# Performance work log

Measured on AMD Instinct MI355X. Metric: run time of the kernel, lower is better.

The kernel has to match this reference:

```python
import jax, jax.numpy as jnp
import numpy as np


def setup_inputs() -> dict:
    key = jax.random.key(0)
    k_z, k_cb = jax.random.split(key)
    B, S, D, K = 8, 4096, 256, 8192
    z = jax.random.normal(k_z, (B, S, D), dtype=jnp.float32)
    codebook = jax.random.normal(k_cb, (K, D), dtype=jnp.float32)
    return {"z": z, "codebook": codebook}


def reference(z, codebook):
    """BaseVectorQuantizer.get_quants with distance_type='square',
    padding_idx=-1 (disabled), prob_decay=0 (deterministic argmin).

    z: (B, S, D); codebook: (K, D).
    Returns (embedding (B, S, D), q_indices (B, S, 1)).

    Squared L2 distance uses the ||z||^2 + ||e||^2 - 2 z e^T expansion
    (same math as the broadcasted (z - e)^2 sum, but GEMM-based).
    """
    B, S, D = z.shape
    zf = z.reshape(-1, D)                               # (N, D), N = B*S
    z_sq = jnp.sum(zf * zf, axis=-1, keepdims=True)     # (N, 1)
    e_sq = jnp.sum(codebook * codebook, axis=-1)        # (K,)
    # (N, K) squared distances
    dist = z_sq + e_sq[None, :] - 2.0 * jnp.einsum("nd,kd->nk", zf, codebook)
    idx = jnp.argmin(dist, axis=1)                      # (N,)
    embedding = jnp.take(codebook, idx, axis=0).reshape(B, S, D)
    q_indices = idx.reshape(B, S, 1)
    return embedding, q_indices
```

## Files before the change

### kernel.cpp

```cpp
#include <hip/hip_runtime.h>

constexpr int D  = 256;
constexpr int K  = 8192;
constexpr int N  = 32768;

typedef _Float16 f16;
typedef f16   f16x8  __attribute__((ext_vector_type(8)));
typedef float f32x16 __attribute__((ext_vector_type(16)));

__device__ __forceinline__ void gload_lds16(const void* g, void* l) {
    __builtin_amdgcn_global_load_lds(
        (const __attribute__((address_space(1))) unsigned int*)g,
        (__attribute__((address_space(3))) unsigned int*)l,
        16, 0, 0);
}


__global__ void esq_kernel(const float* __restrict__ cb, float* __restrict__ esq) {
    const int lane = threadIdx.x & 63;
    const int code = (int)((blockIdx.x * (size_t)blockDim.x + threadIdx.x) >> 6);
    const float4 v = *reinterpret_cast<const float4*>(cb + (size_t)code * D + lane * 4);
    float s = v.x * v.x + v.y * v.y + v.z * v.z + v.w * v.w;
    #pragma unroll
    for (int m = 32; m >= 1; m >>= 1) s += __shfl_xor(s, m);
    if (lane == 0) esq[code] = s;
}

__global__ void cvt_t(const float* __restrict__ cb, f16* __restrict__ cbt) {
    const int g    = blockIdx.x * 256 + threadIdx.x;
    const int s    = g >> 13;
    const int code = g & 8191;
    const float* src = cb + (size_t)code * D + (s & 31) * 8;
    const float4 a  = *reinterpret_cast<const float4*>(src);
    const float4 b2 = *reinterpret_cast<const float4*>(src + 4);
    const float vf[8] = {a.x, a.y, a.z, a.w, b2.x, b2.y, b2.z, b2.w};
    f16x8 o;
    if (s < 32) {
        #pragma unroll
        for (int e = 0; e < 8; ++e) o[e] = (f16)vf[e];
    } else {
        #pragma unroll
        for (int e = 0; e < 8; ++e) {
            f16 h = (f16)vf[e];
            o[e] = (f16)((vf[e] - (float)h) * 1024.0f);
        }
    }
    *reinterpret_cast<f16x8*>(cbt + ((size_t)s * 8192 + code) * 8) = o;
}

__launch_bounds__(256, 2)
__global__ void vq32(const float* __restrict__ z, const f16* __restrict__ cbt,
                     const float* __restrict__ esq,
                     float* __restrict__ wsv, int* __restrict__ wsi) {
    __shared__ f16 buf[2][16384];

    const int tid  = threadIdx.x;
    const int w    = tid >> 6;
    const int l    = tid & 63;
    const int cid  = l & 31;
    const int half = l >> 5;
    const int rg    = blockIdx.x >> 1;
    const int kh    = blockIdx.x & 1;
    const int kbase = kh * 4096;
    const size_t wrow0 = (size_t)rg * 128 + w * 32;

    f16x8 zh[16], zl[16];
    {
        const float* zr = z + (wrow0 + cid) * D + half * 8;
        #pragma unroll
        for (int u = 0; u < 16; ++u) {
            float4 a  = *reinterpret_cast<const float4*>(zr + u * 16);
            float4 b2 = *reinterpret_cast<const float4*>(zr + u * 16 + 4);
            float vf[8] = {a.x, a.y, a.z, a.w, b2.x, b2.y, b2.z, b2.w};
            f16x8 h, lo;
            #pragma unroll
            for (int e = 0; e < 8; ++e) {
                f16 hh = (f16)vf[e];
                h[e]  = hh;
                lo[e] = (f16)((vf[e] - (float)hh) * 1024.0f);
            }
            zh[u] = h; zl[u] = lo;
        }
    }

    float minv[16];
    int   mini[16];
    #pragma unroll
    for (int g = 0; g < 16; ++g) { minv[g] = 3.0e38f; mini[g] = 0; }

    f32x16 accA = (f32x16)0.0f, accB = (f32x16)0.0f;

    #pragma unroll
    for (int j = 0; j < 8; ++j) {
        const int s = w * 16 + 2 * j + half;
        gload_lds16(cbt + ((size_t)s * 8192 + kbase + cid) * 8,
                    &buf[0][(w * 16 + 2 * j) * 256]);
    }
    __syncthreads();

    for (int kt = 0; kt < 128; ++kt) {
        const int  b        = kt & 1;
        const bool haveNext = (kt < 127);

        if (haveNext) {
            const int k0n = kbase + (kt + 1) * 32;
            #pragma unroll
            for (int j = 0; j < 8; ++j) {
                const int s = w * 16 + 2 * j + half;
                gload_lds16(cbt + ((size_t)s * 8192 + k0n + cid) * 8,
                            &buf[b ^ 1][(w * 16 + 2 * j) * 256]);
            }
        }
        const float es = esq[kbase + kt * 32 + cid];

        const f16* Bp = &buf[b][0];
        __builtin_amdgcn_s_setprio(1);
        #pragma unroll
        for (int u = 0; u < 16; ++u) {
            f16x8 beh = *reinterpret_cast<const f16x8*>(Bp + ((2 * u + half) * 32 + cid) * 8);
            f16x8 bel = *reinterpret_cast<const f16x8*>(Bp + ((32 + 2 * u + half) * 32 + cid) * 8);
            accA = __builtin_amdgcn_mfma_f32_32x32x16_f16(zh[u], beh, accA, 0, 0, 0);
            accB = __builtin_amdgcn_mfma_f32_32x32x16_f16(zl[u], beh, accB, 0, 0, 0);
            accB = __builtin_amdgcn_mfma_f32_32x32x16_f16(zh[u], bel, accB, 0, 0, 0);
        }
        __builtin_amdgcn_s_setprio(0);

        const int c0 = kbase + kt * 32 + cid;
        #pragma unroll
        for (int g = 0; g < 16; ++g) {
            float d = fmaf(accB[g], 0.0009765625f, accA[g]);
            float s = fmaf(-2.0f, d, es);
            if (s < minv[g]) { minv[g] = s; mini[g] = c0; }
        }
        accA = (f32x16)0.0f; accB = (f32x16)0.0f;

        if (haveNext) __syncthreads();
    }

    #pragma unroll
    for (int g = 0; g < 16; ++g) {
        float v   = minv[g];
        int   idx = mini[g];
        #pragma unroll
        for (int m = 1; m < 32; m <<= 1) {
            float ov = __shfl_xor(v, m);
            int   oi = __shfl_xor(idx, m);
            if (ov < v || (ov == v && oi < idx)) { v = ov; idx = oi; }
        }
        const size_t row = wrow0 + (g & 3) + 8 * (g >> 2) + 4 * half;
        if (cid == 0) {
            wsv[(size_t)kh * N + row] = v;
            wsi[(size_t)kh * N + row] = idx;
        }
    }
}

__global__ void merge_gather(const float* __restrict__ wsv, const int* __restrict__ wsi,
                             const float* __restrict__ cb, float* __restrict__ out) {
    const int t   = threadIdx.x;
    const int r   = blockIdx.x * 16 + (t >> 4);
    const int l16 = t & 15;
    const float v0 = wsv[r], v1 = wsv[N + r];
    const int   i0 = wsi[r], i1 = wsi[N + r];
    const int idx = (v1 < v0) ? i1 : i0;
    if (l16 == 0) out[(size_t)N * D + r] = (float)idx;
    const float4* src = reinterpret_cast<const float4*>(cb + (size_t)idx * D);
    float4*       dst = reinterpret_cast<float4*>(out + (size_t)r * D);
    #pragma unroll
    for (int it = 0; it < 4; ++it) dst[l16 + 16 * it] = src[l16 + 16 * it];
}

constexpr int BM = 128, BN = 128, TD = 32, ZS = 260, CS = 36;

__launch_bounds__(256)
__global__ void vq_kernel(const float* __restrict__ z, const float* __restrict__ cb,
                          const float* __restrict__ esq, float* __restrict__ out) {
    __shared__ float zs[BM * ZS];
    __shared__ float cs[BN * CS];
    const int tid = threadIdx.x;
    const int tx  = tid & 15;
    const int ty  = tid >> 4;
    const size_t row0 = (size_t)blockIdx.x * BM;
    #pragma unroll
    for (int i = 0; i < 32; ++i) {
        int f  = tid + i * 256;
        int r  = f >> 6;
        int c4 = (f & 63) * 4;
        *reinterpret_cast<float4*>(&zs[r * ZS + c4]) =
            *reinterpret_cast<const float4*>(z + (row0 + r) * D + c4);
    }
    float minv[8]; int mini[8];
    #pragma unroll
    for (int i = 0; i < 8; ++i) { minv[i] = 3.4e38f; mini[i] = 0; }
    for (int k0 = 0; k0 < K; k0 += BN) {
        float acc[8][8];
        #pragma unroll
        for (int i = 0; i < 8; ++i)
            #pragma unroll
            for (int j = 0; j < 8; ++j) acc[i][j] = 0.0f;
        for (int dc = 0; dc < D; dc += TD) {
            __syncthreads();
            int c = tid >> 3, c4 = (tid & 7) * 4;
            #pragma unroll
            for (int i = 0; i < 4; ++i)
                *reinterpret_cast<float4*>(&cs[(c + 32 * i) * CS + c4]) =
                    *reinterpret_cast<const float4*>(cb + (size_t)(k0 + c + 32 * i) * D + dc + c4);
            __syncthreads();
            for (int d4 = 0; d4 < TD; d4 += 4) {
                float4 a[8], b[8];
                #pragma unroll
                for (int i = 0; i < 8; ++i)
                    a[i] = *reinterpret_cast<const float4*>(&zs[(ty + 16 * i) * ZS + dc + d4]);
                #pragma unroll
                for (int j = 0; j < 8; ++j)
                    b[j] = *reinterpret_cast<const float4*>(&cs[(tx + 16 * j) * CS + d4]);
                #pragma unroll
                for (int i = 0; i < 8; ++i)
                    #pragma unroll
                    for (int j = 0; j < 8; ++j)
                        acc[i][j] += a[i].x * b[j].x + a[i].y * b[j].y
                                   + a[i].z * b[j].z + a[i].w * b[j].w;
            }
        }
        #pragma unroll
        for (int j = 0; j < 8; ++j) {
            int code = k0 + tx + 16 * j;
            float es = esq[code];
            #pragma unroll
            for (int i = 0; i < 8; ++i) {
                float score = fmaf(-2.0f, acc[i][j], es);
                if (score < minv[i]) { minv[i] = score; mini[i] = code; }
            }
        }
    }
    float* out_idx = out + (size_t)N * D;
    #pragma unroll
    for (int i = 0; i < 8; ++i) {
        float v = minv[i]; int idx = mini[i];
        #pragma unroll
        for (int m = 1; m < 16; m <<= 1) {
            float ov = __shfl_xor(v, m);
            int   oi = __shfl_xor(idx, m);
            if (ov < v || (ov == v && oi < idx)) { v = ov; idx = oi; }
        }
        size_t row = row0 + ty + 16 * i;
        if (tx == 0) out_idx[row] = (float)idx;
        const float4* src = reinterpret_cast<const float4*>(cb + (size_t)idx * D);
        float4*       dst = reinterpret_cast<float4*>(out + row * D);
        #pragma unroll
        for (int t = 0; t < 4; ++t) dst[tx + 16 * t] = src[tx + 16 * t];
    }
}

extern "C" void kernel_launch(void* const* d_in, const int* in_sizes, int n_in,
                              void* d_out, int out_size, void* d_ws, size_t ws_size,
                              hipStream_t stream) {
    const float* z   = (const float*)d_in[0];
    const float* cb  = (const float*)d_in[1];
    float*       out = (float*)d_out;

    const size_t cbt_bytes = (size_t)K * 512 * sizeof(f16);
    const size_t esq_bytes = (size_t)K * sizeof(float);
    const size_t wsv_bytes = (size_t)2 * N * sizeof(float);
    const size_t wsi_bytes = (size_t)2 * N * sizeof(int);
    const size_t need = cbt_bytes + esq_bytes + wsv_bytes + wsi_bytes;

    if (ws_size >= need) {
        char* p = (char*)d_ws;
        f16*   cbt  = (f16*)p;                 p += cbt_bytes;
        float* esqp = (float*)p;               p += esq_bytes;
        float* wsv  = (float*)p;               p += wsv_bytes;
        int*   wsi  = (int*)p;
        esq_kernel<<<(K * 64) / 256, 256, 0, stream>>>(cb, esqp);
        cvt_t<<<(K * 64) / 256, 256, 0, stream>>>(cb, cbt);
        vq32<<<512, 256, 0, stream>>>(z, cbt, esqp, wsv, wsi);
        merge_gather<<<N / 16, 256, 0, stream>>>(wsv, wsi, cb, out);
    } else {
        float* esqp = (float*)d_ws;
        esq_kernel<<<(K * 64) / 256, 256, 0, stream>>>(cb, esqp);
        vq_kernel<<<N / BM, 256, 0, stream>>>(z, cb, esqp, out);
    }
}
```

Measured before the change: 368.9 us.

## Give each wave two 32-row tiles to double LDS fragment reuse

Halves the block to two waves, each computing a 64-row by 32-code tile with two sets of accumulators so every codebook fragment read from LDS feeds six MFMAs instead of three. The block barrier is moved before the argmin epilogue so the next prefetch can overlap it, and the priority hints are removed. The cost is roughly doubled register use per wave (z fragments, accumulators, running minima), which cuts occupancy to about one wave per SIMD and reduces latency hiding.

```diff
diff --git a/kernel.cpp b/kernel.cpp
--- a/kernel.cpp
+++ b/kernel.cpp
@@ -48,7 +48,7 @@
     *reinterpret_cast<f16x8*>(cbt + ((size_t)s * 8192 + code) * 8) = o;
 }
 
-__launch_bounds__(256, 2)
+__launch_bounds__(128, 1)
 __global__ void vq32(const float* __restrict__ z, const f16* __restrict__ cbt,
                      const float* __restrict__ esq,
                      float* __restrict__ wsv, int* __restrict__ wsi) {
@@ -62,11 +62,12 @@
     const int rg    = blockIdx.x >> 1;
     const int kh    = blockIdx.x & 1;
     const int kbase = kh * 4096;
-    const size_t wrow0 = (size_t)rg * 128 + w * 32;
-
-    f16x8 zh[16], zl[16];
-    {
-        const float* zr = z + (wrow0 + cid) * D + half * 8;
+    const size_t wrow0 = (size_t)rg * 128 + w * 64;
+
+    f16x8 zh0[16], zl0[16], zh1[16], zl1[16];
+    #pragma unroll
+    for (int t = 0; t < 2; ++t) {
+        const float* zr = z + (wrow0 + t * 32 + cid) * D + half * 8;
         #pragma unroll
         for (int u = 0; u < 16; ++u) {
             float4 a  = *reinterpret_cast<const float4*>(zr + u * 16);
@@ -79,22 +80,27 @@
                 h[e]  = hh;
                 lo[e] = (f16)((vf[e] - (float)hh) * 1024.0f);
             }
-            zh[u] = h; zl[u] = lo;
-        }
-    }
-
-    float minv[16];
-    int   mini[16];
-    #pragma unroll
-    for (int g = 0; g < 16; ++g) { minv[g] = 3.0e38f; mini[g] = 0; }
-
-    f32x16 accA = (f32x16)0.0f, accB = (f32x16)0.0f;
-
-    #pragma unroll
-    for (int j = 0; j < 8; ++j) {
-        const int s = w * 16 + 2 * j + half;
+            if (t == 0) { zh0[u] = h; zl0[u] = lo; }
+            else        { zh1[u] = h; zl1[u] = lo; }
+        }
+    }
+
+    float minv0[16], minv1[16];
+    int   mini0[16], mini1[16];
+    #pragma unroll
+    for (int g = 0; g < 16; ++g) {
+        minv0[g] = 3.0e38f; mini0[g] = 0;
+        minv1[g] = 3.0e38f; mini1[g] = 0;
+    }
+
+    f32x16 accA0 = (f32x16)0.0f, accB0 = (f32x16)0.0f;
+    f32x16 accA1 = (f32x16)0.0f, accB1 = (f32x16)0.0f;
+
+    #pragma unroll
+    for (int j = 0; j < 16; ++j) {
+        const int s = w * 32 + 2 * j + half;
         gload_lds16(cbt + ((size_t)s * 8192 + kbase + cid) * 8,
-                    &buf[0][(w * 16 + 2 * j) * 256]);
+                    &buf[0][(w * 32 + 2 * j) * 256]);
     }
     __syncthreads();
 
@@ -105,52 +111,60 @@
         if (haveNext) {
             const int k0n = kbase + (kt + 1) * 32;
             #pragma unroll
-            for (int j = 0; j < 8; ++j) {
-                const int s = w * 16 + 2 * j + half;
+            for (int j = 0; j < 16; ++j) {
+                const int s = w * 32 + 2 * j + half;
                 gload_lds16(cbt + ((size_t)s * 8192 + k0n + cid) * 8,
-                            &buf[b ^ 1][(w * 16 + 2 * j) * 256]);
+                            &buf[b ^ 1][(w * 32 + 2 * j) * 256]);
             }
         }
         const float es = esq[kbase + kt * 32 + cid];
 
         const f16* Bp = &buf[b][0];
-        __builtin_amdgcn_s_setprio(1);
         #pragma unroll
         for (int u = 0; u < 16; ++u) {
             f16x8 beh = *reinterpret_cast<const f16x8*>(Bp + ((2 * u + half) * 32 + cid) * 8);
             f16x8 bel = *reinterpret_cast<const f16x8*>(Bp + ((32 + 2 * u + half) * 32 + cid) * 8);
-            accA = __builtin_amdgcn_mfma_f32_32x32x16_f16(zh[u], beh, accA, 0, 0, 0);
-            accB = __builtin_amdgcn_mfma_f32_32x32x16_f16(zl[u], beh, accB, 0, 0, 0);
-            accB = __builtin_amdgcn_mfma_f32_32x32x16_f16(zh[u], bel, accB, 0, 0, 0);
-        }
-        __builtin_amdgcn_s_setprio(0);
+            accA0 = __builtin_amdgcn_mfma_f32_32x32x16_f16(zh0[u], beh, accA0, 0, 0, 0);
+            accA1 = __builtin_amdgcn_mfma_f32_32x32x16_f16(zh1[u], beh, accA1, 0, 0, 0);
+            accB0 = __builtin_amdgcn_mfma_f32_32x32x16_f16(zl0[u], beh, accB0, 0, 0, 0);
+            accB1 = __builtin_amdgcn_mfma_f32_32x32x16_f16(zl1[u], beh, accB1, 0, 0, 0);
+            accB0 = __builtin_amdgcn_mfma_f32_32x32x16_f16(zh0[u], bel, accB0, 0, 0, 0);
+            accB1 = __builtin_amdgcn_mfma_f32_32x32x16_f16(zh1[u], bel, accB1, 0, 0, 0);
+        }
+
+        if (haveNext) __syncthreads();
 
         const int c0 = kbase + kt * 32 + cid;
         #pragma unroll
         for (int g = 0; g < 16; ++g) {
-            float d = fmaf(accB[g], 0.0009765625f, accA[g]);
-            float s = fmaf(-2.0f, d, es);
-            if (s < minv[g]) { minv[g] = s; mini[g] = c0; }
-        }
-        accA = (f32x16)0.0f; accB = (f32x16)0.0f;
-
-        if (haveNext) __syncthreads();
-    }
-
-    #pragma unroll
-    for (int g = 0; g < 16; ++g) {
-        float v   = minv[g];
-        int   idx = mini[g];
-        #pragma unroll
-        for (int m = 1; m < 32; m <<= 1) {
-            float ov = __shfl_xor(v, m);
-            int   oi = __shfl_xor(idx, m);
-            if (ov < v || (ov == v && oi < idx)) { v = ov; idx = oi; }
-        }
-        const size_t row = wrow0 + (g & 3) + 8 * (g >> 2) + 4 * half;
-        if (cid == 0) {
-            wsv[(size_t)kh * N + row] = v;
-            wsi[(size_t)kh * N + row] = idx;
+            float d0 = fmaf(accB0[g], 0.0009765625f, accA0[g]);
+            float s0 = fmaf(-2.0f, d0, es);
+            if (s0 < minv0[g]) { minv0[g] = s0; mini0[g] = c0; }
+            float d1 = fmaf(accB1[g], 0.0009765625f, accA1[g]);
+            float s1 = fmaf(-2.0f, d1, es);
+            if (s1 < minv1[g]) { minv1[g] = s1; mini1[g] = c0; }
+        }
+        accA0 = (f32x16)0.0f; accB0 = (f32x16)0.0f;
+        accA1 = (f32x16)0.0f; accB1 = (f32x16)0.0f;
+    }
+
+    #pragma unroll
+    for (int t = 0; t < 2; ++t) {
+        #pragma unroll
+        for (int g = 0; g < 16; ++g) {
+            float v   = t ? minv1[g] : minv0[g];
+            int   idx = t ? mini1[g] : mini0[g];
+            #pragma unroll
+            for (int m = 1; m < 32; m <<= 1) {
+                float ov = __shfl_xor(v, m);
+                int   oi = __shfl_xor(idx, m);
+                if (ov < v || (ov == v && oi < idx)) { v = ov; idx = oi; }
+            }
+            const size_t row = wrow0 + t * 32 + (g & 3) + 8 * (g >> 2) + 4 * half;
+            if (cid == 0) {
+                wsv[(size_t)kh * N + row] = v;
+                wsi[(size_t)kh * N + row] = idx;
+            }
         }
     }
 }
@@ -273,7 +287,7 @@
         int*   wsi  = (int*)p;
         esq_kernel<<<(K * 64) / 256, 256, 0, stream>>>(cb, esqp);
         cvt_t<<<(K * 64) / 256, 256, 0, stream>>>(cb, cbt);
-        vq32<<<512, 256, 0, stream>>>(z, cbt, esqp, wsv, wsi);
+        vq32<<<512, 128, 0, stream>>>(z, cbt, esqp, wsv, wsi);
         merge_gather<<<N / 16, 256, 0, stream>>>(wsv, wsi, cb, out);
     } else {
         float* esqp = (float*)d_ws;
```

New measurement: 391.7 us. 1.06x slower.

## Double-buffer MFMA accumulators to overlap argmin epilogue with next tile

Applied to the files above, without the earlier changes.

Uses two pairs of accumulators so the distance/argmin update for tile k-1 runs while the MFMAs for tile k are issued, instead of serialising the epilogue after each tile's matrix work. The loop is manually unrolled by two with a lambda, and the final tile's epilogue is drained after the loop. It also gives half of the blocks a higher wave priority to stagger scheduling between co-resident blocks. The extra 32 accumulator registers raise VGPR pressure, which could cause spills or hurt occupancy under the 2-blocks launch bound.

```diff
diff --git a/kernel.cpp b/kernel.cpp
--- a/kernel.cpp
+++ b/kernel.cpp
@@ -13,6 +13,13 @@
         (const __attribute__((address_space(1))) unsigned int*)g,
         (__attribute__((address_space(3))) unsigned int*)l,
         16, 0, 0);
+}
+
+__device__ __forceinline__ void prio_hi(int pb) {
+    if (pb) __builtin_amdgcn_s_setprio(2); else __builtin_amdgcn_s_setprio(1);
+}
+__device__ __forceinline__ void prio_lo(int pb) {
+    if (pb) __builtin_amdgcn_s_setprio(1); else __builtin_amdgcn_s_setprio(0);
 }
 
 
@@ -62,6 +69,7 @@
     const int rg    = blockIdx.x >> 1;
     const int kh    = blockIdx.x & 1;
     const int kbase = kh * 4096;
+    const int pb    = (blockIdx.x >> 8) & 1;
     const size_t wrow0 = (size_t)rg * 128 + w * 32;
 
     f16x8 zh[16], zl[16];
@@ -88,7 +96,11 @@
     #pragma unroll
     for (int g = 0; g < 16; ++g) { minv[g] = 3.0e38f; mini[g] = 0; }
 
-    f32x16 accA = (f32x16)0.0f, accB = (f32x16)0.0f;
+    f32x16 accA0 = (f32x16)0.0f, accB0 = (f32x16)0.0f;
+    f32x16 accA1 = (f32x16)0.0f, accB1 = (f32x16)0.0f;
+
+    float es_prev = 0.0f;
+    int   c0_prev = 0;
 
     #pragma unroll
     for (int j = 0; j < 8; ++j) {
@@ -98,43 +110,55 @@
     }
     __syncthreads();
 
-    for (int kt = 0; kt < 128; ++kt) {
-        const int  b        = kt & 1;
-        const bool haveNext = (kt < 127);
-
-        if (haveNext) {
-            const int k0n = kbase + (kt + 1) * 32;
+    auto tile = [&](int KT, f32x16& AC, f32x16& BC, f32x16& AP, f32x16& BPk,
+                    int FIRST, int LAST, const f16* Brd, f16* Bwr) {
+        if (!LAST) {
+            const int k0n = kbase + (KT + 1) * 32;
             #pragma unroll
             for (int j = 0; j < 8; ++j) {
                 const int s = w * 16 + 2 * j + half;
                 gload_lds16(cbt + ((size_t)s * 8192 + k0n + cid) * 8,
-                            &buf[b ^ 1][(w * 16 + 2 * j) * 256]);
-            }
-        }
-        const float es = esq[kbase + kt * 32 + cid];
-
-        const f16* Bp = &buf[b][0];
-        __builtin_amdgcn_s_setprio(1);
+                            Bwr + (w * 16 + 2 * j) * 256);
+            }
+        }
+        const float es_c = esq[kbase + KT * 32 + cid];
+        const int   c0_c = kbase + KT * 32 + cid;
+        if (!FIRST) {
+            #pragma unroll
+            for (int g = 0; g < 16; ++g) {
+                float d = fmaf(BPk[g], 0.0009765625f, AP[g]);
+                float s = fmaf(-2.0f, d, es_prev);
+                if (s < minv[g]) { minv[g] = s; mini[g] = c0_prev; }
+            }
+            AP  = (f32x16)0.0f;
+            BPk = (f32x16)0.0f;
+        }
+        prio_hi(pb);
         #pragma unroll
         for (int u = 0; u < 16; ++u) {
-            f16x8 beh = *reinterpret_cast<const f16x8*>(Bp + ((2 * u + half) * 32 + cid) * 8);
-            f16x8 bel = *reinterpret_cast<const f16x8*>(Bp + ((32 + 2 * u + half) * 32 + cid) * 8);
-            accA = __builtin_amdgcn_mfma_f32_32x32x16_f16(zh[u], beh, accA, 0, 0, 0);
-            accB = __builtin_amdgcn_mfma_f32_32x32x16_f16(zl[u], beh, accB, 0, 0, 0);
-            accB = __builtin_amdgcn_mfma_f32_32x32x16_f16(zh[u], bel, accB, 0, 0, 0);
-        }
-        __builtin_amdgcn_s_setprio(0);
-
-        const int c0 = kbase + kt * 32 + cid;
-        #pragma unroll
-        for (int g = 0; g < 16; ++g) {
-            float d = fmaf(accB[g], 0.0009765625f, accA[g]);
-            float s = fmaf(-2.0f, d, es);
-            if (s < minv[g]) { minv[g] = s; mini[g] = c0; }
-        }
-        accA = (f32x16)0.0f; accB = (f32x16)0.0f;
-
-        if (haveNext) __syncthreads();
+            f16x8 beh = *reinterpret_cast<const f16x8*>(Brd + ((2 * u + half) * 32 + cid) * 8);
+            f16x8 bel = *reinterpret_cast<const f16x8*>(Brd + ((32 + 2 * u + half) * 32 + cid) * 8);
+            AC = __builtin_amdgcn_mfma_f32_32x32x16_f16(zh[u], beh, AC, 0, 0, 0);
+            BC = __builtin_amdgcn_mfma_f32_32x32x16_f16(zl[u], beh, BC, 0, 0, 0);
+            BC = __builtin_amdgcn_mfma_f32_32x32x16_f16(zh[u], bel, BC, 0, 0, 0);
+        }
+        prio_lo(pb);
+        es_prev = es_c; c0_prev = c0_c;
+        if (!LAST) __syncthreads();
+    };
+
+    tile(0, accA0, accB0, accA1, accB1, 1, 0, &buf[0][0], &buf[1][0]);
+    for (int kt2 = 0; kt2 < 63; ++kt2) {
+        tile(2 * kt2 + 1, accA1, accB1, accA0, accB0, 0, 0, &buf[1][0], &buf[0][0]);
+        tile(2 * kt2 + 2, accA0, accB0, accA1, accB1, 0, 0, &buf[0][0], &buf[1][0]);
+    }
+    tile(127, accA1, accB1, accA0, accB0, 0, 1, &buf[1][0], &buf[0][0]);
+
+    #pragma unroll
+    for (int g = 0; g < 16; ++g) {
+        float d = fmaf(accB1[g], 0.0009765625f, accA1[g]);
+        float s = fmaf(-2.0f, d, es_prev);
+        if (s < minv[g]) { minv[g] = s; mini[g] = c0_prev; }
     }
 
     #pragma unroll
```

After: 658.3 us. +78.4%, slower.

## Screen with single fp16 GEMM, rescue near-tie rows with split-precision recompute

Applied to the files above, without the earlier changes.

The main pass now uses a single fp16 MFMA per tile instead of the hi/lo split's three, tracking both the best and second-best distance per row across three codebook chunks. Rows whose top-two gap is below a fixed margin are appended to a list via an atomic counter. A rescue kernel recomputes those rows with the full hi/lo split-precision GEMM across 32 codebook slices, and a fixup kernel merges the results and gathers the chosen codes. This cuts most of the MFMA work but adds kernels, atomics and a fixed-size rescue launch, and correctness depends on the margin covering fp16 error and the flagged count staying under the cap.

```diff
diff --git a/kernel.cpp b/kernel.cpp
--- a/kernel.cpp
+++ b/kernel.cpp
@@ -3,6 +3,9 @@
 constexpr int D  = 256;
 constexpr int K  = 8192;
 constexpr int N  = 32768;
+constexpr float TMARG = 0.5f;
+constexpr int  CAP  = 16384;
+constexpr int  RCH  = 32;
 
 typedef _Float16 f16;
 typedef f16   f16x8  __attribute__((ext_vector_type(8)));
@@ -16,7 +19,9 @@
 }
 
 
-__global__ void esq_kernel(const float* __restrict__ cb, float* __restrict__ esq) {
+__global__ void esq_kernel(const float* __restrict__ cb, float* __restrict__ esq,
+                           int* __restrict__ cnt) {
+    if (blockIdx.x == 0 && threadIdx.x == 0) *cnt = 0;
     const int lane = threadIdx.x & 63;
     const int code = (int)((blockIdx.x * (size_t)blockDim.x + threadIdx.x) >> 6);
     const float4 v = *reinterpret_cast<const float4*>(cb + (size_t)code * D + lane * 4);
@@ -48,25 +53,175 @@
     *reinterpret_cast<f16x8*>(cbt + ((size_t)s * 8192 + code) * 8) = o;
 }
 
-__launch_bounds__(256, 2)
-__global__ void vq32(const float* __restrict__ z, const f16* __restrict__ cbt,
-                     const float* __restrict__ esq,
-                     float* __restrict__ wsv, int* __restrict__ wsi) {
-    __shared__ f16 buf[2][16384];
+__launch_bounds__(256, 3)
+__global__ void vq16a(const float* __restrict__ z, const f16* __restrict__ cbt,
+                      const float* __restrict__ esq,
+                      float* __restrict__ wv1, int* __restrict__ wi1,
+                      float* __restrict__ wv2) {
+    __shared__ f16 buf[2][8192];
 
     const int tid  = threadIdx.x;
     const int w    = tid >> 6;
     const int l    = tid & 63;
     const int cid  = l & 31;
     const int half = l >> 5;
-    const int rg    = blockIdx.x >> 1;
-    const int kh    = blockIdx.x & 1;
-    const int kbase = kh * 4096;
+    const int kc   = blockIdx.x % 3;
+    const int rg   = blockIdx.x / 3;
+    const int kc0  = kc * 2720;
+    const int NT   = (kc == 2) ? 86 : 85;
     const size_t wrow0 = (size_t)rg * 128 + w * 32;
+
+    f16x8 zh[16];
+    {
+        const float* zr = z + (wrow0 + cid) * D + half * 8;
+        #pragma unroll
+        for (int u = 0; u < 16; ++u) {
+            float4 a  = *reinterpret_cast<const float4*>(zr + u * 16);
+            float4 b2 = *reinterpret_cast<const float4*>(zr + u * 16 + 4);
+            float vf[8] = {a.x, a.y, a.z, a.w, b2.x, b2.y, b2.z, b2.w};
+            f16x8 h;
+            #pragma unroll
+            for (int e = 0; e < 8; ++e) h[e] = (f16)vf[e];
+            zh[u] = h;
+        }
+    }
+
+    float minv[16], mnv2[16];
+    int   mini[16];
+    #pragma unroll
+    for (int g = 0; g < 16; ++g) { minv[g] = 3.0e38f; mnv2[g] = 3.0e38f; mini[g] = 0; }
+
+    f32x16 acc = (f32x16)0.0f;
+
+    #pragma unroll
+    for (int j = 0; j < 4; ++j) {
+        const int s = w * 8 + 2 * j + half;
+        gload_lds16(cbt + ((size_t)s * 8192 + kc0 + cid) * 8,
+                    &buf[0][(w * 8 + 2 * j) * 256]);
+    }
+    __syncthreads();
+
+    for (int kt = 0; kt < NT; ++kt) {
+        const int  b        = kt & 1;
+        const bool haveNext = (kt < NT - 1);
+
+        if (haveNext) {
+            const int k0n = kc0 + (kt + 1) * 32;
+            #pragma unroll
+            for (int j = 0; j < 4; ++j) {
+                const int s = w * 8 + 2 * j + half;
+                gload_lds16(cbt + ((size_t)s * 8192 + k0n + cid) * 8,
+                            &buf[b ^ 1][(w * 8 + 2 * j) * 256]);
+            }
+        }
+        const float es = esq[kc0 + kt * 32 + cid];
+
+        const f16* Bp = &buf[b][0];
+        __builtin_amdgcn_s_setprio(1);
+        #pragma unroll
+        for (int u = 0; u < 16; ++u) {
+            f16x8 beh = *reinterpret_cast<const f16x8*>(Bp + ((2 * u + half) * 32 + cid) * 8);
+            acc = __builtin_amdgcn_mfma_f32_32x32x16_f16(zh[u], beh, acc, 0, 0, 0);
+        }
+        __builtin_amdgcn_s_setprio(0);
+
+        const int c0 = kc0 + kt * 32 + cid;
+        #pragma unroll
+        for (int g = 0; g < 16; ++g) {
+            float s = fmaf(-2.0f, acc[g], es);
+            if (s < minv[g])      { mnv2[g] = minv[g]; minv[g] = s; mini[g] = c0; }
+            else if (s < mnv2[g]) { mnv2[g] = s; }
+        }
+        acc = (f32x16)0.0f;
+
+        if (haveNext) __syncthreads();
+    }
+
+    #pragma unroll
+    for (int g = 0; g < 16; ++g) {
+        float v1 = minv[g], v2 = mnv2[g];
+        int   i1 = mini[g];
+        #pragma unroll
+        for (int m = 1; m < 32; m <<= 1) {
+            float ov1 = __shfl_xor(v1, m);
+            int   oi1 = __shfl_xor(i1, m);
+            float ov2 = __shfl_xor(v2, m);
+            if (ov1 < v1 || (ov1 == v1 && oi1 < i1)) {
+                v2 = fminf(v1, ov2); v1 = ov1; i1 = oi1;
+            } else {
+                v2 = fminf(v2, ov1);
+            }
+        }
+        const size_t row = wrow0 + (g & 3) + 8 * (g >> 2) + 4 * half;
+        if (cid == 0) {
+            wv1[(size_t)kc * N + row] = v1;
+            wi1[(size_t)kc * N + row] = i1;
+            wv2[(size_t)kc * N + row] = v2;
+        }
+    }
+}
+
+__global__ void flagmerge(const float* __restrict__ wv1, const int* __restrict__ wi1,
+                          const float* __restrict__ wv2, const float* __restrict__ cb,
+                          float* __restrict__ out, int* __restrict__ list,
+                          int* __restrict__ cnt) {
+    const int t    = threadIdx.x;
+    const int r    = blockIdx.x * 16 + (t >> 4);
+    const int l16  = t & 15;
+    const int lane = t & 63;
+
+    float v1 = wv1[r], v2 = wv2[r];
+    int   i1 = wi1[r];
+    #pragma unroll
+    for (int c = 1; c < 3; ++c) {
+        const float cv1 = wv1[(size_t)c * N + r];
+        const int   ci1 = wi1[(size_t)c * N + r];
+        const float cv2 = wv2[(size_t)c * N + r];
+        if (cv1 < v1) { v2 = fminf(v1, cv2); v1 = cv1; i1 = ci1; }
+        else          { v2 = fminf(v2, cv1); }
+    }
+    const bool flagged = (v2 - v1) < TMARG;
+
+    int pos = -1;
+    if (flagged && l16 == 0) pos = atomicAdd(cnt, 1);
+    pos = __shfl(pos, (lane >> 4) << 4);
+
+    if (flagged && pos < CAP) {
+        if (l16 == 0) list[pos] = r;
+        return;
+    }
+    if (l16 == 0) out[(size_t)N * D + r] = (float)i1;
+    const float4* src = reinterpret_cast<const float4*>(cb + (size_t)i1 * D);
+    float4*       dst = reinterpret_cast<float4*>(out + (size_t)r * D);
+    #pragma unroll
+    for (int it = 0; it < 4; ++it) dst[l16 + 16 * it] = src[l16 + 16 * it];
+}
+
+__launch_bounds__(256, 2)
+__global__ void rescue(const float* __restrict__ z, const f16* __restrict__ cbt,
+                       const float* __restrict__ esq, const int* __restrict__ list,
+                       const int* __restrict__ cnt,
+                       float* __restrict__ pv, int* __restrict__ pi) {
+    const int rgi = blockIdx.x >> 5;
+    const int kc  = blockIdx.x & (RCH - 1);
+    const int cc  = min(*cnt, CAP);
+    if (rgi * 128 >= cc) return;
+
+    __shared__ f16 buf[2][16384];
+
+    const int tid  = threadIdx.x;
+    const int w    = tid >> 6;
+    const int l    = tid & 63;
+    const int cid  = l & 31;
+    const int half = l >> 5;
+    const int kb   = kc * 256;
+
+    const int myslot = rgi * 128 + w * 32 + cid;
+    const int lrow   = list[min(myslot, cc - 1)];
 
     f16x8 zh[16], zl[16];
     {
-        const float* zr = z + (wrow0 + cid) * D + half * 8;
+        const float* zr = z + (size_t)lrow * D + half * 8;
         #pragma unroll
         for (int u = 0; u < 16; ++u) {
             float4 a  = *reinterpret_cast<const float4*>(zr + u * 16);
@@ -93,17 +248,17 @@
     #pragma unroll
     for (int j = 0; j < 8; ++j) {
         const int s = w * 16 + 2 * j + half;
-        gload_lds16(cbt + ((size_t)s * 8192 + kbase + cid) * 8,
+        gload_lds16(cbt + ((size_t)s * 8192 + kb + cid) * 8,
                     &buf[0][(w * 16 + 2 * j) * 256]);
     }
     __syncthreads();
 
-    for (int kt = 0; kt < 128; ++kt) {
+    for (int kt = 0; kt < 8; ++kt) {
         const int  b        = kt & 1;
-        const bool haveNext = (kt < 127);
+        const bool haveNext = (kt < 7);
 
         if (haveNext) {
-            const int k0n = kbase + (kt + 1) * 32;
+            const int k0n = kb + (kt + 1) * 32;
             #pragma unroll
             for (int j = 0; j < 8; ++j) {
                 const int s = w * 16 + 2 * j + half;
@@ -111,10 +266,9 @@
                             &buf[b ^ 1][(w * 16 + 2 * j) * 256]);
             }
         }
-        const float es = esq[kbase + kt * 32 + cid];
+        const float es = esq[kb + kt * 32 + cid];
 
         const f16* Bp = &buf[b][0];
-        __builtin_amdgcn_s_setprio(1);
         #pragma unroll
         for (int u = 0; u < 16; ++u) {
             f16x8 beh = *reinterpret_cast<const f16x8*>(Bp + ((2 * u + half) * 32 + cid) * 8);
@@ -123,9 +277,8 @@
             accB = __builtin_amdgcn_mfma_f32_32x32x16_f16(zl[u], beh, accB, 0, 0, 0);
             accB = __builtin_amdgcn_mfma_f32_32x32x16_f16(zh[u], bel, accB, 0, 0, 0);
         }
-        __builtin_amdgcn_s_setprio(0);
-
-        const int c0 = kbase + kt * 32 + cid;
+
+        const int c0 = kb + kt * 32 + cid;
         #pragma unroll
         for (int g = 0; g < 16; ++g) {
             float d = fmaf(accB[g], 0.0009765625f, accA[g]);
@@ -147,30 +300,48 @@
             int   oi = __shfl_xor(idx, m);
             if (ov < v || (ov == v && oi < idx)) { v = ov; idx = oi; }
         }
-        const size_t row = wrow0 + (g & 3) + 8 * (g >> 2) + 4 * half;
-        if (cid == 0) {
-            wsv[(size_t)kh * N + row] = v;
-            wsi[(size_t)kh * N + row] = idx;
-        }
-    }
-}
-
-__global__ void merge_gather(const float* __restrict__ wsv, const int* __restrict__ wsi,
-                             const float* __restrict__ cb, float* __restrict__ out) {
+        const int pos = rgi * 128 + w * 32 + (g & 3) + 8 * (g >> 2) + 4 * half;
+        if (cid == 0 && pos < cc) {
+            pv[(size_t)pos * RCH + kc] = v;
+            pi[(size_t)pos * RCH + kc] = idx;
+        }
+    }
+}
+
+__global__ void fixup(const int* __restrict__ list, const int* __restrict__ cnt,
+                      const float* __restrict__ pv, const int* __restrict__ pi,
+                      const float* __restrict__ cb, float* __restrict__ out) {
     const int t   = threadIdx.x;
-    const int r   = blockIdx.x * 16 + (t >> 4);
+    const int p   = blockIdx.x * 16 + (t >> 4);
     const int l16 = t & 15;
-    const float v0 = wsv[r], v1 = wsv[N + r];
-    const int   i0 = wsi[r], i1 = wsi[N + r];
-    const int idx = (v1 < v0) ? i1 : i0;
-    if (l16 == 0) out[(size_t)N * D + r] = (float)idx;
+    const int cc  = min(*cnt, CAP);
+    if (p >= cc) return;
+    const int row = list[p];
+    float v   = pv[(size_t)p * RCH];
+    int   idx = pi[(size_t)p * RCH];
+    #pragma unroll
+    for (int c = 1; c < RCH; ++c) {
+        const float cv = pv[(size_t)p * RCH + c];
+        if (cv < v) { v = cv; idx = pi[(size_t)p * RCH + c]; }
+    }
+    if (l16 == 0) out[(size_t)N * D + row] = (float)idx;
     const float4* src = reinterpret_cast<const float4*>(cb + (size_t)idx * D);
-    float4*       dst = reinterpret_cast<float4*>(out + (size_t)r * D);
+    float4*       dst = reinterpret_cast<float4*>(out + (size_t)row * D);
     #pragma unroll
     for (int it = 0; it < 4; ++it) dst[l16 + 16 * it] = src[l16 + 16 * it];
 }
 
 constexpr int BM = 128, BN = 128, TD = 32, ZS = 260, CS = 36;
+
+__global__ void esq_only(const float* __restrict__ cb, float* __restrict__ esq) {
+    const int lane = threadIdx.x & 63;
+    const int code = (int)((blockIdx.x * (size_t)blockDim.x + threadIdx.x) >> 6);
+    const float4 v = *reinterpret_cast<const float4*>(cb + (size_t)code * D + lane * 4);
+    float s = v.x * v.x + v.y * v.y + v.z * v.z + v.w * v.w;
+    #pragma unroll
+    for (int m = 32; m >= 1; m >>= 1) s += __shfl_xor(s, m);
+    if (lane == 0) esq[code] = s;
+}
 
 __launch_bounds__(256)
 __global__ void vq_kernel(const float* __restrict__ z, const float* __restrict__ cb,
@@ -259,25 +430,36 @@
     const float* cb  = (const float*)d_in[1];
     float*       out = (float*)d_out;
 
-    const size_t cbt_bytes = (size_t)K * 512 * sizeof(f16);
-    const size_t esq_bytes = (size_t)K * sizeof(float);
-    const size_t wsv_bytes = (size_t)2 * N * sizeof(float);
-    const size_t wsi_bytes = (size_t)2 * N * sizeof(int);
-    const size_t need = cbt_bytes + esq_bytes + wsv_bytes + wsi_bytes;
+    const size_t cbt_b  = (size_t)K * 512 * sizeof(f16);
+    const size_t esq_b  = (size_t)K * sizeof(float);
+    const size_t wv_b   = (size_t)3 * N * sizeof(float);
+    const size_t wi_b   = (size_t)3 * N * sizeof(int);
+    const size_t list_b = (size_t)CAP * sizeof(int);
+    const size_t pv_b   = (size_t)CAP * RCH * sizeof(float);
+    const size_t pi_b   = (size_t)CAP * RCH * sizeof(int);
+    const size_t need = cbt_b + esq_b + 2 * wv_b + wi_b + list_b + pv_b + pi_b + 256;
 
     if (ws_size >= need) {
         char* p = (char*)d_ws;
-        f16*   cbt  = (f16*)p;                 p += cbt_bytes;
-        float* esqp = (float*)p;               p += esq_bytes;
-        float* wsv  = (float*)p;               p += wsv_bytes;
-        int*   wsi  = (int*)p;
-        esq_kernel<<<(K * 64) / 256, 256, 0, stream>>>(cb, esqp);
+        f16*   cbt  = (f16*)p;     p += cbt_b;
+        float* esqp = (float*)p;   p += esq_b;
+        float* wv1  = (float*)p;   p += wv_b;
+        int*   wi1  = (int*)p;     p += wi_b;
+        float* wv2  = (float*)p;   p += wv_b;
+        int*   list = (int*)p;     p += list_b;
+        float* pv   = (float*)p;   p += pv_b;
+        int*   pi   = (int*)p;     p += pi_b;
+        int*   cnt  = (int*)p;
+
+        esq_kernel<<<(K * 64) / 256, 256, 0, stream>>>(cb, esqp, cnt);
         cvt_t<<<(K * 64) / 256, 256, 0, stream>>>(cb, cbt);
-        vq32<<<512, 256, 0, stream>>>(z, cbt, esqp, wsv, wsi);
-        merge_gather<<<N / 16, 256, 0, stream>>>(wsv, wsi, cb, out);
+        vq16a<<<768, 256, 0, stream>>>(z, cbt, esqp, wv1, wi1, wv2);
+        flagmerge<<<N / 16, 256, 0, stream>>>(wv1, wi1, wv2, cb, out, list, cnt);
+        rescue<<<(CAP / 128) * RCH, 256, 0, stream>>>(z, cbt, esqp, list, cnt, pv, pi);
+        fixup<<<CAP / 16, 256, 0, stream>>>(list, cnt, pv, pi, cb, out);
     } else {
         float* esqp = (float*)d_ws;
-        esq_kernel<<<(K * 64) / 256, 256, 0, stream>>>(cb, esqp);
+        esq_only<<<(K * 64) / 256, 256, 0, stream>>>(cb, esqp);
         vq_kernel<<<N / BM, 256, 0, stream>>>(z, cb, esqp, out);
     }
 }
```

Result: slower. 449.4 us (+21.8%).
